# Kernel optimization log

Hardware: AMD Instinct MI355X
Metric: run time of the kernel (lower is better)

The kernel has to match this reference:

```python
import jax, jax.numpy as jnp
import numpy as np

N = 50000
E = 800000
D_IN, D_HID, D_OUT = 128, 128, 64


def _glorot(key, shape):
    fan_in, fan_out = shape[1], shape[0]
    lim = np.sqrt(6.0 / (fan_in + fan_out))
    return jax.random.uniform(key, shape, jnp.float32, -lim, lim)


def setup_inputs() -> dict:
    key = jax.random.key(0)
    ks = jax.random.split(key, 12)
    x = jax.random.normal(ks[0], (N, D_IN), jnp.float32)
    edge_index = jax.random.randint(ks[1], (2, E), 0, N, jnp.int32)
    edge_attr = jax.random.uniform(ks[2], (E,), jnp.float32)
    return {
        "x": x,
        "edge_index": edge_index,
        "edge_attr": edge_attr,
        # conv1: in -> hidden
        "W1_rel": _glorot(ks[3], (D_HID, D_IN)),
        "b1_rel": jnp.zeros((D_HID,), jnp.float32),
        "W1_root": _glorot(ks[4], (D_HID, D_IN)),
        # conv_mu: hidden -> out
        "Wmu_rel": _glorot(ks[5], (D_OUT, D_HID)),
        "bmu_rel": jnp.zeros((D_OUT,), jnp.float32),
        "Wmu_root": _glorot(ks[6], (D_OUT, D_HID)),
        # conv_logvar: hidden -> out
        "Wlv_rel": _glorot(ks[7], (D_OUT, D_HID)),
        "blv_rel": jnp.zeros((D_OUT,), jnp.float32),
        "Wlv_root": _glorot(ks[8], (D_OUT, D_HID)),
    }


def sage_conv(x, src, dst, ew, W_rel, b_rel, W_root, n_nodes):
    # message: edge_weight * x_j  (gather from source nodes)
    msg = x[src] * ew[:, None]                                   # [E, d]
    agg = jax.ops.segment_sum(msg, dst, num_segments=n_nodes)    # [N, d]
    cnt = jax.ops.segment_sum(jnp.ones_like(ew), dst, num_segments=n_nodes)
    mean = agg / jnp.maximum(cnt, 1.0)[:, None]                  # scatter-mean
    return mean @ W_rel.T + b_rel + x @ W_root.T


def reference(x, edge_index, edge_attr, W1_rel, b1_rel, W1_root,
              Wmu_rel, bmu_rel, Wmu_root, Wlv_rel, blv_rel, Wlv_root):
    src, dst = edge_index[0], edge_index[1]
    h = jax.nn.elu(sage_conv(x, src, dst, edge_attr, W1_rel, b1_rel, W1_root, N))
    mu = sage_conv(h, src, dst, edge_attr, Wmu_rel, bmu_rel, Wmu_root, N)
    logvar = sage_conv(h, src, dst, edge_attr, Wlv_rel, blv_rel, Wlv_root, N)
    return mu, logvar
```

## Files before the change

### kernel.cpp

```cpp
#include <hip/hip_runtime.h>
#include <hip/hip_bf16.h>
#include <math.h>

#define NNODES 50000
#define NEDGES 800000
#define NRANGE 6250
#define NC     64
#define CHUNK_E (NEDGES / NC)
#define NSLICE 4
#define SLICE_E (CHUNK_E / NSLICE)

using short8 = __attribute__((ext_vector_type(8))) short;
using f32x4  = __attribute__((ext_vector_type(4))) float;
typedef unsigned long long u64;

__device__ __forceinline__ short f2bf(float f) {
    __hip_bfloat16 h = __float2bfloat16(f);
    return *reinterpret_cast<short*>(&h);
}


__global__ __launch_bounds__(512)
void prep_kernel(const float* __restrict__ x, __hip_bfloat16* __restrict__ xb,
                 const float* __restrict__ w0, const float* __restrict__ w1,
                 const float* __restrict__ w2, const float* __restrict__ w3,
                 const float* __restrict__ w4, const float* __restrict__ w5,
                 __hip_bfloat16* __restrict__ Wb,
                 const int* __restrict__ dst, unsigned int* __restrict__ partial,
                 unsigned char* __restrict__ rank8) {
    __shared__ unsigned int hist[NNODES / 4];
    int b = blockIdx.x;
    int tid = threadIdx.x;
    if (b < 64) {
        int c = b;
        for (int i = tid; i < NNODES / 4; i += 512) hist[i] = 0;
        __syncthreads();
        int base = c * CHUNK_E;
        for (int e = base + tid; e < base + CHUNK_E; e += 512) {
            int d = dst[e];
            int sh = 8 * (d & 3);
            unsigned int old = atomicAdd(&hist[d >> 2], 1u << sh);
            rank8[e] = (unsigned char)((old >> sh) & 0xffu);
        }
        __syncthreads();
        unsigned int* outp = partial + (size_t)c * (NNODES / 4);
        for (int i = tid; i < NNODES / 4; i += 512) outp[i] = hist[i];
    } else if (b < 1627) {
        int i = (b - 64) * 512 + tid;
        if (i < 800000) {
            const float4* p = (const float4*)x + (size_t)i * 2;
            float4 a = p[0], c4 = p[1];
            short8 o;
            o[0] = f2bf(a.x); o[1] = f2bf(a.y); o[2] = f2bf(a.z); o[3] = f2bf(a.w);
            o[4] = f2bf(c4.x); o[5] = f2bf(c4.y); o[6] = f2bf(c4.z); o[7] = f2bf(c4.w);
            *reinterpret_cast<short8*>((short*)xb + (size_t)i * 8) = o;
        }
    } else {
        int i = (b - 1627) * 512 + tid;
        const float* src; int off;
        if      (i < 16384) { src = w0; off = 0; }
        else if (i < 32768) { src = w1; off = 16384; }
        else if (i < 40960) { src = w2; off = 32768; }
        else if (i < 49152) { src = w3; off = 40960; }
        else if (i < 57344) { src = w4; off = 49152; }
        else                { src = w5; off = 57344; }
        Wb[i] = __float2bfloat16(src[i - off]);
    }
}


__global__ __launch_bounds__(1024)
void scan1_kernel(const unsigned int* __restrict__ partial,
                  unsigned char* __restrict__ cbase,
                  int* __restrict__ excl, int* __restrict__ bsum) {
    __shared__ int sdata[1024];
    int tid = threadIdx.x;
    int n = blockIdx.x * 1024 + tid;
    int deg = 0;
    if (n < NNODES) {
        int sh = 8 * (n & 3);
        int idx = n >> 2;
        unsigned int packed = 0;
        unsigned int* cbout = (unsigned int*)(cbase + (size_t)n * NC);
#pragma unroll 4
        for (int c = 0; c < NC; ++c) {
            unsigned int w = partial[(size_t)c * (NNODES / 4) + idx];
            unsigned int cc = (w >> sh) & 0xffu;
            packed |= ((unsigned int)(deg & 0xff)) << (8 * (c & 3));
            deg += (int)cc;
            if ((c & 3) == 3) { cbout[c >> 2] = packed; packed = 0; }
        }
    }
    sdata[tid] = deg;
    __syncthreads();
    for (int off = 1; off < 1024; off <<= 1) {
        int t = (tid >= off) ? sdata[tid - off] : 0;
        __syncthreads();
        sdata[tid] += t;
        __syncthreads();
    }
    if (n < NNODES) excl[n] = sdata[tid] - deg;
    if (tid == 1023) bsum[blockIdx.x] = sdata[1023];
}

__global__ __launch_bounds__(64)
void scan2_kernel(int* __restrict__ bsum, int nb) {
    int lane = threadIdx.x;
    int v = (lane < nb) ? bsum[lane] : 0;
    int incl = v;
    for (int off = 1; off < 64; off <<= 1) {
        int t = __shfl_up(incl, off);
        if (lane >= off) incl += t;
    }
    if (lane < nb) bsum[lane] = incl - v;
    if (lane == 63) bsum[nb] = incl;
}


__global__ __launch_bounds__(256)
void fill_kernel(const int* __restrict__ src, const int* __restrict__ dst,
                 const float* __restrict__ ew,
                 const int* __restrict__ excl, const int* __restrict__ bsum,
                 const unsigned char* __restrict__ cbase,
                 const unsigned char* __restrict__ rank8,
                 u64* __restrict__ edges) {
    int b = blockIdx.x;
    int r = b & 7;
    int t = b >> 3;
    int c = t & (NC - 1);
    int s = t >> 6;
    int lo = r * NRANGE;
    int base = c * CHUNK_E + s * SLICE_E;
    int end = base + SLICE_E;
    for (int e = base + threadIdx.x; e < end; e += 256) {
        int d = dst[e];
        unsigned int dl = (unsigned int)(d - lo);
        if (dl < NRANGE) {
            int slot = excl[d] + bsum[d >> 10] + (int)cbase[(size_t)d * NC + c] + (int)rank8[e];
            u64 pack = ((u64)(unsigned int)__float_as_int(ew[e]) << 32) | (unsigned int)src[e];
            edges[slot] = pack;
        }
    }
}


__device__ __forceinline__ void gstep(u64 e, const unsigned int* __restrict__ Fb,
                                      int lane, float& ax, float& ay) {
    unsigned int v = Fb[(size_t)(unsigned int)e * 64 + lane];
    float w = __uint_as_float((unsigned int)(e >> 32));
    ax += __uint_as_float(v << 16) * w;
    ay += __uint_as_float(v & 0xffff0000u) * w;
}

__global__ __launch_bounds__(256)
void gather_mean_kernel(const unsigned int* __restrict__ Fb,
                        const int* __restrict__ excl, const int* __restrict__ bsum,
                        const u64* __restrict__ edges,
                        unsigned int* __restrict__ outb,
                        int n_nodes, int E) {
    int node = (blockIdx.x * blockDim.x + threadIdx.x) >> 6;
    int lane = threadIdx.x & 63;
    if (node >= n_nodes) return;
    int beg = excl[node] + bsum[node >> 10];
    int end = (node + 1 < n_nodes) ? (excl[node + 1] + bsum[(node + 1) >> 10]) : E;
    beg = __builtin_amdgcn_readfirstlane(beg);
    end = __builtin_amdgcn_readfirstlane(end);

    float ax[8], ay[8];
#pragma unroll
    for (int j = 0; j < 8; ++j) { ax[j] = 0.f; ay[j] = 0.f; }

    int s = beg;
    for (; s + 8 <= end; s += 8) {
        u64 e[8];
#pragma unroll
        for (int j = 0; j < 8; ++j) e[j] = __builtin_nontemporal_load(edges + s + j);
#pragma unroll
        for (int j = 0; j < 8; ++j) gstep(e[j], Fb, lane, ax[j], ay[j]);
    }
    if (s + 4 <= end) {
        u64 e[4];
#pragma unroll
        for (int j = 0; j < 4; ++j) e[j] = __builtin_nontemporal_load(edges + s + j);
#pragma unroll
        for (int j = 0; j < 4; ++j) gstep(e[j], Fb, lane, ax[j], ay[j]);
        s += 4;
    }
    if (s + 2 <= end) {
        u64 e0 = __builtin_nontemporal_load(edges + s);
        u64 e1 = __builtin_nontemporal_load(edges + s + 1);
        gstep(e0, Fb, lane, ax[0], ay[0]);
        gstep(e1, Fb, lane, ax[1], ay[1]);
        s += 2;
    }
    if (s < end) {
        u64 e0 = __builtin_nontemporal_load(edges + s);
        gstep(e0, Fb, lane, ax[0], ay[0]);
    }
#pragma unroll
    for (int j = 4; j < 8; ++j) { ax[j - 4] += ax[j]; ay[j - 4] += ay[j]; }
    float axs = (ax[0] + ax[1]) + (ax[2] + ax[3]);
    float ays = (ay[0] + ay[1]) + (ay[2] + ay[3]);
    float inv = 1.f / fmaxf((float)(end - beg), 1.f);
    unsigned int lo = (unsigned int)(unsigned short)f2bf(axs * inv);
    unsigned int hi = (unsigned int)(unsigned short)f2bf(ays * inv);
    outb[(size_t)node * 64 + lane] = lo | (hi << 16);
}


__global__ __launch_bounds__(256)
void linear1_mfma(const __hip_bfloat16* __restrict__ Ab1,
                  const __hip_bfloat16* __restrict__ Ab2,
                  const __hip_bfloat16* __restrict__ Wb,
                  const float* __restrict__ bias,
                  __hip_bfloat16* __restrict__ outb,
                  int n_nodes) {
    int wid  = threadIdx.x >> 6;
    int lane = threadIdx.x & 63;
    int nodeBase = blockIdx.x * 64 + wid * 16;
    int m  = lane & 15;
    int kq = lane >> 4;
    int node = nodeBase + m;
    int nodeC = (node < n_nodes) ? node : (n_nodes - 1);

    short8 a1[4], a2[4];
    const short* A1p = (const short*)Ab1 + (size_t)nodeC * 128 + kq * 8;
    const short* A2p = (const short*)Ab2 + (size_t)nodeC * 128 + kq * 8;
#pragma unroll
    for (int kk = 0; kk < 4; ++kk) {
        a1[kk] = *(const short8*)(A1p + kk * 32);
        a2[kk] = *(const short8*)(A2p + kk * 32);
    }
    const short* Wrel  = (const short*)Wb;
    const short* Wroot = (const short*)Wb + 16384;

#pragma unroll
    for (int c = 0; c < 8; ++c) {
        f32x4 acc = {0.f, 0.f, 0.f, 0.f};
        const short* b1p = Wrel  + (size_t)(c * 16 + m) * 128 + kq * 8;
        const short* b2p = Wroot + (size_t)(c * 16 + m) * 128 + kq * 8;
#pragma unroll
        for (int kk = 0; kk < 4; ++kk) {
            short8 bw1 = *(const short8*)(b1p + kk * 32);
            acc = __builtin_amdgcn_mfma_f32_16x16x32_bf16(a1[kk], bw1, acc, 0, 0, 0);
            short8 bw2 = *(const short8*)(b2p + kk * 32);
            acc = __builtin_amdgcn_mfma_f32_16x16x32_bf16(a2[kk], bw2, acc, 0, 0, 0);
        }
        int col = c * 16 + m;
        float b = bias[col];
#pragma unroll
        for (int i = 0; i < 4; ++i) {
            int gn = nodeBase + kq * 4 + i;
            if (gn < n_nodes) {
                float v = acc[i] + b;
                v = (v > 0.f) ? v : expm1f(v);
                outb[(size_t)gn * 128 + col] = __float2bfloat16(v);
            }
        }
    }
}

__global__ __launch_bounds__(256)
void linear2_mfma(const __hip_bfloat16* __restrict__ Ab1,
                  const __hip_bfloat16* __restrict__ Ab2,
                  const __hip_bfloat16* __restrict__ Wb,
                  const float* __restrict__ bmu, const float* __restrict__ blv,
                  float* __restrict__ out,
                  int n_nodes) {
    int wid  = threadIdx.x >> 6;
    int lane = threadIdx.x & 63;
    int nodeBase = blockIdx.x * 64 + wid * 16;
    int m  = lane & 15;
    int kq = lane >> 4;
    int node = nodeBase + m;
    int nodeC = (node < n_nodes) ? node : (n_nodes - 1);

    short8 a1[4], a2[4];
    const short* A1p = (const short*)Ab1 + (size_t)nodeC * 128 + kq * 8;
    const short* A2p = (const short*)Ab2 + (size_t)nodeC * 128 + kq * 8;
#pragma unroll
    for (int kk = 0; kk < 4; ++kk) {
        a1[kk] = *(const short8*)(A1p + kk * 32);
        a2[kk] = *(const short8*)(A2p + kk * 32);
    }
    const short* WmuR = (const short*)Wb + 32768;
    const short* WmuT = (const short*)Wb + 40960;
    const short* WlvR = (const short*)Wb + 49152;
    const short* WlvT = (const short*)Wb + 57344;

#pragma unroll
    for (int c = 0; c < 4; ++c) {
        f32x4 accMu = {0.f, 0.f, 0.f, 0.f};
        f32x4 accLv = {0.f, 0.f, 0.f, 0.f};
        size_t wrow = (size_t)(c * 16 + m) * 128 + kq * 8;
#pragma unroll
        for (int kk = 0; kk < 4; ++kk) {
            short8 bm1 = *(const short8*)(WmuR + wrow + kk * 32);
            accMu = __builtin_amdgcn_mfma_f32_16x16x32_bf16(a1[kk], bm1, accMu, 0, 0, 0);
            short8 bm2 = *(const short8*)(WmuT + wrow + kk * 32);
            accMu = __builtin_amdgcn_mfma_f32_16x16x32_bf16(a2[kk], bm2, accMu, 0, 0, 0);
            short8 bl1 = *(const short8*)(WlvR + wrow + kk * 32);
            accLv = __builtin_amdgcn_mfma_f32_16x16x32_bf16(a1[kk], bl1, accLv, 0, 0, 0);
            short8 bl2 = *(const short8*)(WlvT + wrow + kk * 32);
            accLv = __builtin_amdgcn_mfma_f32_16x16x32_bf16(a2[kk], bl2, accLv, 0, 0, 0);
        }
        int col = c * 16 + m;
        float bm = bmu[col], bl = blv[col];
#pragma unroll
        for (int i = 0; i < 4; ++i) {
            int gn = nodeBase + kq * 4 + i;
            if (gn < n_nodes) {
                out[(size_t)gn * 64 + col] = accMu[i] + bm;
                out[(size_t)NNODES * 64 + (size_t)gn * 64 + col] = accLv[i] + bl;
            }
        }
    }
}

extern "C" void kernel_launch(void* const* d_in, const int* in_sizes, int n_in,
                              void* d_out, int out_size, void* d_ws, size_t ws_size,
                              hipStream_t stream) {
    const float* x        = (const float*)d_in[0];
    const int*   eidx     = (const int*)d_in[1];
    const float* eattr    = (const float*)d_in[2];
    const float* W1_rel   = (const float*)d_in[3];
    const float* b1_rel   = (const float*)d_in[4];
    const float* W1_root  = (const float*)d_in[5];
    const float* Wmu_rel  = (const float*)d_in[6];
    const float* bmu_rel  = (const float*)d_in[7];
    const float* Wmu_root = (const float*)d_in[8];
    const float* Wlv_rel  = (const float*)d_in[9];
    const float* blv_rel  = (const float*)d_in[10];
    const float* Wlv_root = (const float*)d_in[11];
    float* out = (float*)d_out;

    const int N = NNODES, E = NEDGES;
    const int nb = (N + 1023) / 1024;
    const int* src = eidx;
    const int* dst = eidx + E;

    char* ws = (char*)d_ws;
    size_t off = 0;
    int* excl = (int*)(ws + off); off += (size_t)N * 4;
    int* bsum = (int*)(ws + off); off += 256;
    off = (off + 63) & ~(size_t)63;
    unsigned int* partial = (unsigned int*)(ws + off); off += (size_t)NC * (N / 4) * 4;
    unsigned char* cbase  = (unsigned char*)(ws + off); off += (size_t)N * NC;
    unsigned char* rank8  = (unsigned char*)(ws + off); off += (size_t)E;
    off = (off + 63) & ~(size_t)63;
    u64* edges = (u64*)(ws + off); off += (size_t)E * 8;
    __hip_bfloat16* xb    = (__hip_bfloat16*)(ws + off); off += (size_t)N * 128 * 2;
    __hip_bfloat16* meanb = (__hip_bfloat16*)(ws + off); off += (size_t)N * 128 * 2;
    __hip_bfloat16* hb    = (__hip_bfloat16*)(ws + off); off += (size_t)N * 128 * 2;
    __hip_bfloat16* Wb    = (__hip_bfloat16*)(ws + off); off += 65536 * 2;

    prep_kernel<<<1755, 512, 0, stream>>>(x, xb, W1_rel, W1_root, Wmu_rel, Wmu_root,
                                          Wlv_rel, Wlv_root, Wb, dst, partial, rank8);
    scan1_kernel<<<nb, 1024, 0, stream>>>(partial, cbase, excl, bsum);
    scan2_kernel<<<1, 64, 0, stream>>>(bsum, nb);
    fill_kernel<<<NC * 8 * NSLICE, 256, 0, stream>>>(src, dst, eattr, excl, bsum,
                                                     cbase, rank8, edges);

    gather_mean_kernel<<<(N * 64 + 255) / 256, 256, 0, stream>>>(
        (const unsigned int*)xb, excl, bsum, edges, (unsigned int*)meanb, N, E);
    linear1_mfma<<<(N + 63) / 64, 256, 0, stream>>>(meanb, xb, Wb, b1_rel, hb, N);
    gather_mean_kernel<<<(N * 64 + 255) / 256, 256, 0, stream>>>(
        (const unsigned int*)hb, excl, bsum, edges, (unsigned int*)meanb, N, E);
    linear2_mfma<<<(N + 63) / 64, 256, 0, stream>>>(meanb, hb, Wb, bmu_rel, blv_rel, out, N);
}
```

Baseline: 203.6 us.

## Fuse neighbor gather-mean with MFMA linear layers via shared-memory staging

Merges each gather_mean kernel with the following MFMA linear kernel. Each 256-thread block now gathers means for 16 nodes (4 per wave), stages them in LDS, then the four waves split the output columns of the MFMA. This removes the bf16 mean buffer write/read and two kernel launches. In exchange each block handles far fewer nodes for the GEMM, reloads weights per 16 nodes, adds a block-wide barrier that leaves waves with light nodes idle behind the heaviest one, and drops bounds checks by relying on N being divisible by 16.

```diff
diff --git a/kernel.cpp b/kernel.cpp
--- a/kernel.cpp
+++ b/kernel.cpp
@@ -152,24 +152,12 @@
     ay += __uint_as_float(v & 0xffff0000u) * w;
 }
 
-__global__ __launch_bounds__(256)
-void gather_mean_kernel(const unsigned int* __restrict__ Fb,
-                        const int* __restrict__ excl, const int* __restrict__ bsum,
-                        const u64* __restrict__ edges,
-                        unsigned int* __restrict__ outb,
-                        int n_nodes, int E) {
-    int node = (blockIdx.x * blockDim.x + threadIdx.x) >> 6;
-    int lane = threadIdx.x & 63;
-    if (node >= n_nodes) return;
-    int beg = excl[node] + bsum[node >> 10];
-    int end = (node + 1 < n_nodes) ? (excl[node + 1] + bsum[(node + 1) >> 10]) : E;
-    beg = __builtin_amdgcn_readfirstlane(beg);
-    end = __builtin_amdgcn_readfirstlane(end);
-
+__device__ __forceinline__ unsigned int gather_node(const unsigned int* __restrict__ Fb,
+                                                    const u64* __restrict__ edges,
+                                                    int beg, int end, int lane) {
     float ax[8], ay[8];
 #pragma unroll
     for (int j = 0; j < 8; ++j) { ax[j] = 0.f; ay[j] = 0.f; }
-
     int s = beg;
     for (; s + 8 <= end; s += 8) {
         u64 e[8];
@@ -204,38 +192,53 @@
     float inv = 1.f / fmaxf((float)(end - beg), 1.f);
     unsigned int lo = (unsigned int)(unsigned short)f2bf(axs * inv);
     unsigned int hi = (unsigned int)(unsigned short)f2bf(ays * inv);
-    outb[(size_t)node * 64 + lane] = lo | (hi << 16);
-}
-
+    return lo | (hi << 16);
+}
+
+
+#define SMW 20
 
 __global__ __launch_bounds__(256)
-void linear1_mfma(const __hip_bfloat16* __restrict__ Ab1,
-                  const __hip_bfloat16* __restrict__ Ab2,
-                  const __hip_bfloat16* __restrict__ Wb,
-                  const float* __restrict__ bias,
-                  __hip_bfloat16* __restrict__ outb,
-                  int n_nodes) {
+void fused1_kernel(const unsigned int* __restrict__ Fb,
+                   const __hip_bfloat16* __restrict__ xb,
+                   const int* __restrict__ excl, const int* __restrict__ bsum,
+                   const u64* __restrict__ edges,
+                   const __hip_bfloat16* __restrict__ Wb,
+                   const float* __restrict__ bias,
+                   __hip_bfloat16* __restrict__ outb,
+                   int E) {
+    __shared__ unsigned int smean[4][16][SMW];
     int wid  = threadIdx.x >> 6;
     int lane = threadIdx.x & 63;
-    int nodeBase = blockIdx.x * 64 + wid * 16;
+    int nodeBase = blockIdx.x * 16;
+
+    for (int q = 0; q < 4; ++q) {
+        int nodeLocal = wid * 4 + q;
+        int node = nodeBase + nodeLocal;
+        int beg = excl[node] + bsum[node >> 10];
+        int end = (node + 1 < NNODES) ? (excl[node + 1] + bsum[(node + 1) >> 10]) : E;
+        beg = __builtin_amdgcn_readfirstlane(beg);
+        end = __builtin_amdgcn_readfirstlane(end);
+        unsigned int mv = gather_node(Fb, edges, beg, end, lane);
+        smean[lane >> 4][nodeLocal][lane & 15] = mv;
+    }
+    __syncthreads();
+
     int m  = lane & 15;
     int kq = lane >> 4;
-    int node = nodeBase + m;
-    int nodeC = (node < n_nodes) ? node : (n_nodes - 1);
-
     short8 a1[4], a2[4];
-    const short* A1p = (const short*)Ab1 + (size_t)nodeC * 128 + kq * 8;
-    const short* A2p = (const short*)Ab2 + (size_t)nodeC * 128 + kq * 8;
+    const short* A2p = (const short*)xb + (size_t)(nodeBase + m) * 128 + kq * 8;
 #pragma unroll
     for (int kk = 0; kk < 4; ++kk) {
-        a1[kk] = *(const short8*)(A1p + kk * 32);
+        a1[kk] = *(const short8*)((const short*)&smean[kk][m][kq * 4]);
         a2[kk] = *(const short8*)(A2p + kk * 32);
     }
     const short* Wrel  = (const short*)Wb;
     const short* Wroot = (const short*)Wb + 16384;
 
 #pragma unroll
-    for (int c = 0; c < 8; ++c) {
+    for (int cc = 0; cc < 2; ++cc) {
+        int c = wid * 2 + cc;
         f32x4 acc = {0.f, 0.f, 0.f, 0.f};
         const short* b1p = Wrel  + (size_t)(c * 16 + m) * 128 + kq * 8;
         const short* b2p = Wroot + (size_t)(c * 16 + m) * 128 + kq * 8;
@@ -251,36 +254,46 @@
 #pragma unroll
         for (int i = 0; i < 4; ++i) {
             int gn = nodeBase + kq * 4 + i;
-            if (gn < n_nodes) {
-                float v = acc[i] + b;
-                v = (v > 0.f) ? v : expm1f(v);
-                outb[(size_t)gn * 128 + col] = __float2bfloat16(v);
-            }
+            float v = acc[i] + b;
+            v = (v > 0.f) ? v : expm1f(v);
+            outb[(size_t)gn * 128 + col] = __float2bfloat16(v);
         }
     }
 }
 
 __global__ __launch_bounds__(256)
-void linear2_mfma(const __hip_bfloat16* __restrict__ Ab1,
-                  const __hip_bfloat16* __restrict__ Ab2,
-                  const __hip_bfloat16* __restrict__ Wb,
-                  const float* __restrict__ bmu, const float* __restrict__ blv,
-                  float* __restrict__ out,
-                  int n_nodes) {
+void fused2_kernel(const unsigned int* __restrict__ Fb,
+                   const __hip_bfloat16* __restrict__ hb,
+                   const int* __restrict__ excl, const int* __restrict__ bsum,
+                   const u64* __restrict__ edges,
+                   const __hip_bfloat16* __restrict__ Wb,
+                   const float* __restrict__ bmu, const float* __restrict__ blv,
+                   float* __restrict__ out,
+                   int E) {
+    __shared__ unsigned int smean[4][16][SMW];
     int wid  = threadIdx.x >> 6;
     int lane = threadIdx.x & 63;
-    int nodeBase = blockIdx.x * 64 + wid * 16;
+    int nodeBase = blockIdx.x * 16;
+
+    for (int q = 0; q < 4; ++q) {
+        int nodeLocal = wid * 4 + q;
+        int node = nodeBase + nodeLocal;
+        int beg = excl[node] + bsum[node >> 10];
+        int end = (node + 1 < NNODES) ? (excl[node + 1] + bsum[(node + 1) >> 10]) : E;
+        beg = __builtin_amdgcn_readfirstlane(beg);
+        end = __builtin_amdgcn_readfirstlane(end);
+        unsigned int mv = gather_node(Fb, edges, beg, end, lane);
+        smean[lane >> 4][nodeLocal][lane & 15] = mv;
+    }
+    __syncthreads();
+
     int m  = lane & 15;
     int kq = lane >> 4;
-    int node = nodeBase + m;
-    int nodeC = (node < n_nodes) ? node : (n_nodes - 1);
-
     short8 a1[4], a2[4];
-    const short* A1p = (const short*)Ab1 + (size_t)nodeC * 128 + kq * 8;
-    const short* A2p = (const short*)Ab2 + (size_t)nodeC * 128 + kq * 8;
+    const short* A2p = (const short*)hb + (size_t)(nodeBase + m) * 128 + kq * 8;
 #pragma unroll
     for (int kk = 0; kk < 4; ++kk) {
-        a1[kk] = *(const short8*)(A1p + kk * 32);
+        a1[kk] = *(const short8*)((const short*)&smean[kk][m][kq * 4]);
         a2[kk] = *(const short8*)(A2p + kk * 32);
     }
     const short* WmuR = (const short*)Wb + 32768;
@@ -288,32 +301,28 @@
     const short* WlvR = (const short*)Wb + 49152;
     const short* WlvT = (const short*)Wb + 57344;
 
-#pragma unroll
-    for (int c = 0; c < 4; ++c) {
-        f32x4 accMu = {0.f, 0.f, 0.f, 0.f};
-        f32x4 accLv = {0.f, 0.f, 0.f, 0.f};
-        size_t wrow = (size_t)(c * 16 + m) * 128 + kq * 8;
-#pragma unroll
-        for (int kk = 0; kk < 4; ++kk) {
-            short8 bm1 = *(const short8*)(WmuR + wrow + kk * 32);
-            accMu = __builtin_amdgcn_mfma_f32_16x16x32_bf16(a1[kk], bm1, accMu, 0, 0, 0);
-            short8 bm2 = *(const short8*)(WmuT + wrow + kk * 32);
-            accMu = __builtin_amdgcn_mfma_f32_16x16x32_bf16(a2[kk], bm2, accMu, 0, 0, 0);
-            short8 bl1 = *(const short8*)(WlvR + wrow + kk * 32);
-            accLv = __builtin_amdgcn_mfma_f32_16x16x32_bf16(a1[kk], bl1, accLv, 0, 0, 0);
-            short8 bl2 = *(const short8*)(WlvT + wrow + kk * 32);
-            accLv = __builtin_amdgcn_mfma_f32_16x16x32_bf16(a2[kk], bl2, accLv, 0, 0, 0);
-        }
-        int col = c * 16 + m;
-        float bm = bmu[col], bl = blv[col];
-#pragma unroll
-        for (int i = 0; i < 4; ++i) {
-            int gn = nodeBase + kq * 4 + i;
-            if (gn < n_nodes) {
-                out[(size_t)gn * 64 + col] = accMu[i] + bm;
-                out[(size_t)NNODES * 64 + (size_t)gn * 64 + col] = accLv[i] + bl;
-            }
-        }
+    int c = wid;
+    f32x4 accMu = {0.f, 0.f, 0.f, 0.f};
+    f32x4 accLv = {0.f, 0.f, 0.f, 0.f};
+    size_t wrow = (size_t)(c * 16 + m) * 128 + kq * 8;
+#pragma unroll
+    for (int kk = 0; kk < 4; ++kk) {
+        short8 bm1 = *(const short8*)(WmuR + wrow + kk * 32);
+        accMu = __builtin_amdgcn_mfma_f32_16x16x32_bf16(a1[kk], bm1, accMu, 0, 0, 0);
+        short8 bm2 = *(const short8*)(WmuT + wrow + kk * 32);
+        accMu = __builtin_amdgcn_mfma_f32_16x16x32_bf16(a2[kk], bm2, accMu, 0, 0, 0);
+        short8 bl1 = *(const short8*)(WlvR + wrow + kk * 32);
+        accLv = __builtin_amdgcn_mfma_f32_16x16x32_bf16(a1[kk], bl1, accLv, 0, 0, 0);
+        short8 bl2 = *(const short8*)(WlvT + wrow + kk * 32);
+        accLv = __builtin_amdgcn_mfma_f32_16x16x32_bf16(a2[kk], bl2, accLv, 0, 0, 0);
+    }
+    int col = c * 16 + m;
+    float bmv = bmu[col], blv_ = blv[col];
+#pragma unroll
+    for (int i = 0; i < 4; ++i) {
+        int gn = nodeBase + kq * 4 + i;
+        out[(size_t)gn * 64 + col] = accMu[i] + bmv;
+        out[(size_t)NNODES * 64 + (size_t)gn * 64 + col] = accLv[i] + blv_;
     }
 }
 
@@ -350,7 +359,6 @@
     off = (off + 63) & ~(size_t)63;
     u64* edges = (u64*)(ws + off); off += (size_t)E * 8;
     __hip_bfloat16* xb    = (__hip_bfloat16*)(ws + off); off += (size_t)N * 128 * 2;
-    __hip_bfloat16* meanb = (__hip_bfloat16*)(ws + off); off += (size_t)N * 128 * 2;
     __hip_bfloat16* hb    = (__hip_bfloat16*)(ws + off); off += (size_t)N * 128 * 2;
     __hip_bfloat16* Wb    = (__hip_bfloat16*)(ws + off); off += 65536 * 2;
 
@@ -361,10 +369,8 @@
     fill_kernel<<<NC * 8 * NSLICE, 256, 0, stream>>>(src, dst, eattr, excl, bsum,
                                                      cbase, rank8, edges);
 
-    gather_mean_kernel<<<(N * 64 + 255) / 256, 256, 0, stream>>>(
-        (const unsigned int*)xb, excl, bsum, edges, (unsigned int*)meanb, N, E);
-    linear1_mfma<<<(N + 63) / 64, 256, 0, stream>>>(meanb, xb, Wb, b1_rel, hb, N);
-    gather_mean_kernel<<<(N * 64 + 255) / 256, 256, 0, stream>>>(
-        (const unsigned int*)hb, excl, bsum, edges, (unsigned int*)meanb, N, E);
-    linear2_mfma<<<(N + 63) / 64, 256, 0, stream>>>(meanb, hb, Wb, bmu_rel, blv_rel, out, N);
-}
+    fused1_kernel<<<N / 16, 256, 0, stream>>>(
+        (const unsigned int*)xb, xb, excl, bsum, edges, Wb, b1_rel, hb, E);
+    fused2_kernel<<<N / 16, 256, 0, stream>>>(
+        (const unsigned int*)hb, hb, excl, bsum, edges, Wb, bmu_rel, blv_rel, out, E);
+}
```

Result: faster. 180.3 us (-11.5%).
